# Optimization experiments

Hardware: AMD Instinct MI355X
Metric: run time of the kernel (lower is better)

The kernel has to match this reference:

```python
import jax, jax.numpy as jnp
import numpy as np

NUM_ORI = 20
DEGREE = 2
EPS = 1e-5

def _gelu(x):
    return jax.nn.gelu(x, approximate=False)

def _poly(x, degree=DEGREE):
    # PolynomialFeatures: concat of tensor powers 1..degree+1 of last dim
    feats = [x]
    cur = x
    for _ in range(degree):
        cur = (cur[..., :, None] * x[..., None, :]).reshape(x.shape[:-1] + (-1,))
        feats.append(cur)
    return jnp.concatenate(feats, axis=-1)

def setup_inputs():
    key = jax.random.key(0)
    ks = jax.random.split(key, 16)
    B, N, O, Cin, C, L = 1, 160, NUM_ORI, 16, 128, 2
    basis = C
    def w(k, shape, fan_in):
        return jax.random.normal(k, shape, jnp.float32) / np.sqrt(fan_in).astype(np.float32)
    return {
        "x": jax.random.normal(ks[0], (B, N, O, Cin), jnp.float32),
        "pos": jax.random.normal(ks[1], (B, N, 2), jnp.float32),
        "bw1": w(ks[2], (14, C), 14), "bb1": jnp.zeros((C,), jnp.float32),
        "bw2": w(ks[3], (C, basis), C), "bb2": jnp.zeros((basis,), jnp.float32),
        "fw1": w(ks[4], (3, C), 3), "fb1": jnp.zeros((C,), jnp.float32),
        "fw2": w(ks[5], (C, basis), C), "fb2": jnp.zeros((basis,), jnp.float32),
        "emb_w": w(ks[6], (Cin, C), Cin),
        "kernel_w": w(ks[7], (L, basis, C), basis),
        "fiber_w": w(ks[8], (L, basis, C), basis),
        "conv_b": jnp.zeros((L, C), jnp.float32),
        "ln_g": jnp.ones((L, C), jnp.float32), "ln_b": jnp.zeros((L, C), jnp.float32),
        "mlp_w1": w(ks[9], (L, C, 4 * C), C), "mlp_b1": jnp.zeros((L, 4 * C), jnp.float32),
        "mlp_w2": w(ks[10], (L, 4 * C, C), 4 * C), "mlp_b2": jnp.zeros((L, C), jnp.float32),
    }

def reference(x, pos, bw1, bb1, bw2, bb2, fw1, fb1, fw2, fb2, emb_w,
              kernel_w, fiber_w, conv_b, ln_g, ln_b, mlp_w1, mlp_b1, mlp_w2, mlp_b2):
    # uniform grid of orientations on the circle (GridGenerator(2, num_ori))
    theta = jnp.arange(NUM_ORI, dtype=jnp.float32) * (2.0 * jnp.pi / NUM_ORI)
    ori = jnp.stack([jnp.cos(theta), jnp.sin(theta)], axis=-1)              # [O,2]
    rel = pos[:, None, :, None, :] - pos[:, :, None, None, :]               # [B,M,N,1,2]
    inv1 = jnp.sum(rel * ori[None, None, None], axis=-1, keepdims=True)     # [B,M,N,O,1]
    inv2 = jnp.linalg.norm(rel - rel * inv1, axis=-1, keepdims=True)        # [B,M,N,O,1]
    spat = jnp.concatenate([inv1, inv2], axis=-1)                           # [B,M,N,O,2]
    kb = _gelu(_gelu(_poly(spat) @ bw1 + bb1) @ bw2 + bb2)                  # [B,M,N,O,basis]
    oi = jnp.sum(ori[:, None] * ori[None], axis=-1, keepdims=True)          # [P,O,1]
    fkb = _gelu(_gelu(_poly(oi) @ fw1 + fb1) @ fw2 + fb2)                   # [P,O,basis]
    h = x @ emb_w                                                           # [B,N,O,C]
    C = emb_w.shape[1]
    for l in range(kernel_w.shape[0]):
        kern = kb @ kernel_w[l]                                             # [B,M,N,O,C]
        fk = fkb @ fiber_w[l]                                               # [P,O,C]
        x1 = jnp.einsum('bnoc,bmnoc->bmoc', h, kern)                        # spatial conv
        x2 = jnp.einsum('bmoc,poc->bmpc', x1, fk) / C + conv_b[l]           # fiber conv (depthwise)
        mu = jnp.mean(x2, axis=-1, keepdims=True)
        var = jnp.var(x2, axis=-1, keepdims=True)
        xn = (x2 - mu) / jnp.sqrt(var + EPS) * ln_g[l] + ln_b[l]            # LayerNorm
        mid = _gelu(xn @ mlp_w1[l] + mlp_b1[l])                             # bottleneck MLP
        h = h + (mid @ mlp_w2[l] + mlp_b2[l])                               # residual (layer_scale=None)
    return h
```

## Files before the change

kernel.cpp:

```cpp
#include <hip/hip_runtime.h>
#include <math.h>

#define NORI 20
#define NPTS 160
#define CDIM 128
#define TWO_PI_OVER_O (6.28318530717958647692f / 20.0f)
#define SW 132
#define SAS 136
#define SCL 256.0f
#define ISCL 0.00390625f

typedef __attribute__((ext_vector_type(8))) _Float16 half8v;
typedef __attribute__((ext_vector_type(4))) float float4v;

__device__ __forceinline__ float vexp2(float x) {
    float r;
    asm("v_exp_f32 %0, %1" : "=v"(r) : "v"(x));
    return r;
}
__device__ __forceinline__ float vsqrt(float x) {
    float r;
    asm("v_sqrt_f32 %0, %1" : "=v"(r) : "v"(x));
    return r;
}

__device__ __forceinline__ float gelu_exact(float x) {
    float t  = 0.70710678118654752440f * x;
    float at = fabsf(t);
    float tau = __builtin_amdgcn_rcpf(fmaf(0.3275911f, at, 1.0f));
    float p = fmaf(1.061405429f, tau, -1.453152027f);
    p = fmaf(p, tau, 1.421413741f);
    p = fmaf(p, tau, -0.284496736f);
    p = fmaf(p, tau, 0.254829592f);
    p = p * tau;
    float e = vexp2(t * t * -1.44269504088896340736f);
    float erf_abs = fmaf(-p, e, 1.0f);
    float hx = 0.5f * x;
    return fmaf(fabsf(hx), erf_abs, hx);
}
__device__ __forceinline__ float4 ld4(const float* p) { return *(const float4*)p; }
__device__ __forceinline__ unsigned short f16b(float f) {
    _Float16 h = (_Float16)f;
    return __builtin_bit_cast(unsigned short, h);
}
__device__ __forceinline__ float f16tof(unsigned short u) {
    return (float)__builtin_bit_cast(_Float16, u);
}
__device__ __forceinline__ unsigned int pkrtz(float a, float b) {
    auto h = __builtin_amdgcn_cvt_pkrtz(a, b);
    return __builtin_bit_cast(unsigned int, h);
}

#define FMA4(d, s, v) { d.x += (s)*(v).x; d.y += (s)*(v).y; d.z += (s)*(v).z; d.w += (s)*(v).w; }
#define GELU4(d) { d.x = gelu_exact(d.x); d.y = gelu_exact(d.y); \
                   d.z = gelu_exact(d.z); d.w = gelu_exact(d.w); }

__global__ __launch_bounds__(128) void fk_kernel(
    const float* __restrict__ fw1, const float* __restrict__ fb1,
    const float* __restrict__ fw2, const float* __restrict__ fb2,
    const float* __restrict__ fiber_w, unsigned short* __restrict__ fk)
{
    __shared__ float s_u[CDIM];
    __shared__ float s_z[CDIM];
    int bid = blockIdx.x;
    int l = bid / 400;
    int rem = bid % 400;
    int p = rem / 20, o = rem % 20;
    int j = threadIdx.x;

    float t = cosf(TWO_PI_OVER_O * (float)(p - o));
    float f1 = t * t, f2 = f1 * t;

    float u = gelu_exact(t * fw1[j] + f1 * fw1[CDIM + j] + f2 * fw1[2 * CDIM + j] + fb1[j]);
    s_u[j] = u;
    __syncthreads();

    float z0 = 0.f, z1 = 0.f, z2 = 0.f, z3 = 0.f;
    for (int i = 0; i < CDIM; i += 4) {
        z0 += s_u[i    ] * fw2[(i    ) * CDIM + j];
        z1 += s_u[i + 1] * fw2[(i + 1) * CDIM + j];
        z2 += s_u[i + 2] * fw2[(i + 2) * CDIM + j];
        z3 += s_u[i + 3] * fw2[(i + 3) * CDIM + j];
    }
    float z = gelu_exact(((z0 + z1) + (z2 + z3)) + fb2[j]);
    s_z[j] = z;
    __syncthreads();

    const float* fw = fiber_w + l * CDIM * CDIM;
    float a0 = 0.f, a1 = 0.f, a2 = 0.f, a3 = 0.f;
    for (int i = 0; i < CDIM; i += 4) {
        a0 += s_z[i    ] * fw[(i    ) * CDIM + j];
        a1 += s_z[i + 1] * fw[(i + 1) * CDIM + j];
        a2 += s_z[i + 2] * fw[(i + 2) * CDIM + j];
        a3 += s_z[i + 3] * fw[(i + 3) * CDIM + j];
    }
    fk[bid * CDIM + j] = f16b((a0 + a1) + (a2 + a3));
}

__global__ __launch_bounds__(128) void h0_kernel(
    const float* __restrict__ x, const float* __restrict__ emb_w,
    float* __restrict__ h)
{
    int row = blockIdx.x;
    int j = threadIdx.x;
    const float* xr = x + row * 16;
    float acc = 0.f;
#pragma unroll
    for (int i = 0; i < 16; ++i) acc += xr[i] * emb_w[i * CDIM + j];
    h[row * CDIM + j] = acc;
}

__global__ __launch_bounds__(128) void wt_kernel(
    const float* __restrict__ bw2, const float* __restrict__ kernel_w,
    unsigned short* __restrict__ wt)
{
    int b = blockIdx.x;
    int mat = b >> 7, c = b & 127;
    const float* src = (mat == 0) ? bw2 : (kernel_w + (mat - 1) * CDIM * CDIM);
    int k = threadIdx.x;
    wt[(mat * CDIM + c) * CDIM + k] = f16b(src[k * CDIM + c]);
}

#define FOR_BANDS(X) X(0) X(1) X(2) X(3) X(4) X(5) X(6) X(7) X(8) X(9)

#define DECL_ACC(B) float4v acc##B = {0.f,0.f,0.f,0.f};

#define LDB(PTR, KT) (*(const half8v*)((PTR) + col0 * CDIM + (KT) * 32 + lh8))

#define LOADB(P, PTR) \
    half8v P##0 = LDB(PTR, 0); \
    half8v P##1 = LDB(PTR, 1); \
    half8v P##2 = LDB(PTR, 2); \
    half8v P##3 = LDB(PTR, 3);

#define G_BAND(B, P) { \
    const unsigned short* ar_ = s_act + (B) * 16 * SAS + abase; \
    half8v a0_ = *(const half8v*)(ar_); \
    half8v a1_ = *(const half8v*)(ar_ + 32); \
    half8v a2_ = *(const half8v*)(ar_ + 64); \
    half8v a3_ = *(const half8v*)(ar_ + 96); \
    acc##B = __builtin_amdgcn_mfma_f32_16x16x32_f16(a0_, P##0, acc##B, 0, 0, 0); \
    acc##B = __builtin_amdgcn_mfma_f32_16x16x32_f16(a1_, P##1, acc##B, 0, 0, 0); \
    acc##B = __builtin_amdgcn_mfma_f32_16x16x32_f16(a2_, P##2, acc##B, 0, 0, 0); \
    acc##B = __builtin_amdgcn_mfma_f32_16x16x32_f16(a3_, P##3, acc##B, 0, 0, 0); }

#define G1(B) G_BAND(B, bwf)
#define G2(B) G_BAND(B, kwf)

#define ZW_BAND(B) { \
    int rb_ = (B) * 16 + lh4; \
    s_act[(rb_ + 0) * SAS + col0] = f16b(gelu_exact(fmaf(SCL, acc##B.x, zb0)) * ISCL); \
    s_act[(rb_ + 1) * SAS + col0] = f16b(gelu_exact(fmaf(SCL, acc##B.y, zb0)) * ISCL); \
    s_act[(rb_ + 2) * SAS + col0] = f16b(gelu_exact(fmaf(SCL, acc##B.z, zb0)) * ISCL); \
    s_act[(rb_ + 3) * SAS + col0] = f16b(gelu_exact(fmaf(SCL, acc##B.w, zb0)) * ISCL); \
    acc##B = vzero; }

#define H_BAND(B) { \
    int nb_ = (B) * 16 + lh4; \
    xacc0 += acc##B.x * hb0[(nb_ + 0) * 2560]; \
    xacc0 += acc##B.y * hb0[(nb_ + 1) * 2560]; \
    xacc0 += acc##B.z * hb0[(nb_ + 2) * 2560]; \
    xacc0 += acc##B.w * hb0[(nb_ + 3) * 2560]; }

__global__ __launch_bounds__(512, 4) void x1_kernel(
    const float* __restrict__ pos, const float* __restrict__ h,
    const float* __restrict__ bw1, const float* __restrict__ bb1,
    const float* __restrict__ bb2,
    const unsigned short* __restrict__ wtb,
    const unsigned short* __restrict__ wtk,
    float* __restrict__ x1)
{
    __shared__ __align__(16) unsigned short s_act[160 * SAS];
    __shared__ float s_bw1[9 * SW];
    __shared__ float s_bb1[CDIM];

    const int tid = threadIdx.x;
    const int rg = tid & 31;
    const int cgv = tid >> 5;
    const int c0u = cgv << 3;

    if (tid < CDIM) {
        const int c = tid;
        s_bw1[0 * SW + c] = bw1[0 * CDIM + c];
        s_bw1[1 * SW + c] = bw1[1 * CDIM + c];
        s_bw1[2 * SW + c] = bw1[2 * CDIM + c];
        s_bw1[3 * SW + c] = bw1[3 * CDIM + c] + bw1[4 * CDIM + c];
        s_bw1[4 * SW + c] = bw1[5 * CDIM + c];
        s_bw1[5 * SW + c] = bw1[6 * CDIM + c];
        s_bw1[6 * SW + c] = bw1[7 * CDIM + c] + bw1[8 * CDIM + c] + bw1[10 * CDIM + c];
        s_bw1[7 * SW + c] = bw1[9 * CDIM + c] + bw1[11 * CDIM + c] + bw1[12 * CDIM + c];
        s_bw1[8 * SW + c] = bw1[13 * CDIM + c];
        s_bb1[c] = bb1[c];
    }

    const int m = blockIdx.x / NORI;
    const int o = blockIdx.x % NORI;
    const float th = TWO_PI_OVER_O * (float)o;
    const float ox = cosf(th), oy = sinf(th);
    const float pmx = pos[2 * m], pmy = pos[2 * m + 1];

    __syncthreads();

#pragma unroll
    for (int rr = 0; rr < 5; ++rr) {
        const int row = rr * 32 + rg;
        float rx = pos[2 * row] - pmx, ry = pos[2 * row + 1] - pmy;
        float ia = rx * ox + ry * oy;
        float ib = vsqrt(rx * rx + ry * ry) * fabsf(1.0f - ia);
        float q2a = ia * ia, q2m = ia * ib, q2b = ib * ib;
        float q3a = q2a * ia, q3m = q2a * ib, q3n = q2m * ib, q3b = q2b * ib;
        float4 ua = ld4(&s_bb1[c0u]);
        float4 ub = ld4(&s_bb1[c0u + 4]);
#define UF(I, S) { float4 wa_ = ld4(&s_bw1[(I) * SW + c0u]); \
                   float4 wb_ = ld4(&s_bw1[(I) * SW + c0u + 4]); \
                   FMA4(ua, S, wa_); FMA4(ub, S, wb_); }
        UF(0, ia) UF(1, ib) UF(2, q2a) UF(3, q2m) UF(4, q2b)
        UF(5, q3a) UF(6, q3m) UF(7, q3n) UF(8, q3b)
#undef UF
        GELU4(ua) GELU4(ub)
        uint4 up;
        up.x = pkrtz(ua.x * ISCL, ua.y * ISCL);
        up.y = pkrtz(ua.z * ISCL, ua.w * ISCL);
        up.z = pkrtz(ub.x * ISCL, ub.y * ISCL);
        up.w = pkrtz(ub.z * ISCL, ub.w * ISCL);
        *(uint4*)&s_act[row * SAS + c0u] = up;
    }

    const int lane = tid & 63;
    const int wv = tid >> 6;
    const int li = lane & 15;
    const int lh = lane >> 4;
    const int lh8 = lh << 3, lh4 = lh << 2;
    const int col0 = wv * 16 + li;
    const int abase = li * SAS + lh8;
    const float4v vzero = {0.f, 0.f, 0.f, 0.f};

    FOR_BANDS(DECL_ACC)
    LOADB(bwf, wtb)
    __syncthreads();

    FOR_BANDS(G1)
    __syncthreads();

    const float zb0 = bb2[col0];
    FOR_BANDS(ZW_BAND)
    LOADB(kwf, wtk)
    __syncthreads();

    FOR_BANDS(G2)

    const float* hb0 = h + o * CDIM + col0;
    float xacc0 = 0.f;
    FOR_BANDS(H_BAND)

    xacc0 += __shfl_xor(xacc0, 16, 64);
    xacc0 += __shfl_xor(xacc0, 32, 64);

    if (lane < 16)
        x1[(m * NORI + o) * CDIM + col0] = xacc0 * SCL;
}

__global__ __launch_bounds__(128) void mlp_kernel(
    const float* __restrict__ x1, const unsigned short* __restrict__ fk_l,
    const float* __restrict__ conv_b, const float* __restrict__ ln_g,
    const float* __restrict__ ln_b,
    const float* __restrict__ w1, const float* __restrict__ b1,
    const float* __restrict__ w2, const float* __restrict__ b2,
    float* __restrict__ h)
{
    __shared__ float s_xn[2][132];
    __shared__ float s_mid[2][520];
    __shared__ float s_s1[2][2], s_sq[2][2];

    const int c = threadIdx.x;
    const int m = blockIdx.x / 10, pg = blockIdx.x % 10;
    const int lane = c & 63, wid = c >> 6;

    float x1v[NORI];
#pragma unroll
    for (int o = 0; o < NORI; ++o) x1v[o] = x1[(m * NORI + o) * CDIM + c];

    float x2v[2];
#pragma unroll
    for (int rr = 0; rr < 2; ++rr) {
        int p = pg * 2 + rr;
        float x2 = 0.f;
#pragma unroll
        for (int o = 0; o < NORI; ++o) x2 += x1v[o] * f16tof(fk_l[(p * NORI + o) * CDIM + c]);
        x2 = x2 * (1.0f / 128.0f) + conv_b[c];
        x2v[rr] = x2;
        float s1 = x2, sq = x2 * x2;
        for (int off = 32; off; off >>= 1) {
            s1 += __shfl_down(s1, off, 64);
            sq += __shfl_down(sq, off, 64);
        }
        if (lane == 0) { s_s1[rr][wid] = s1; s_sq[rr][wid] = sq; }
    }
    __syncthreads();
#pragma unroll
    for (int rr = 0; rr < 2; ++rr) {
        float mu  = (s_s1[rr][0] + s_s1[rr][1]) * (1.0f / 128.0f);
        float var = (s_sq[rr][0] + s_sq[rr][1]) * (1.0f / 128.0f) - mu * mu;
        float xn = (x2v[rr] - mu) * rsqrtf(var + 1e-5f) * ln_g[c] + ln_b[c];
        s_xn[rr][c] = xn;
    }
    __syncthreads();

#pragma unroll
    for (int kq = 0; kq < 4; ++kq) {
        int k = kq * CDIM + c;
        float b = b1[k];
        float ac0 = b, ac1 = b;
        for (int i = 0; i < CDIM; ++i) {
            float w = w1[i * 512 + k];
            ac0 += s_xn[0][i] * w;
            ac1 += s_xn[1][i] * w;
        }
        s_mid[0][k] = gelu_exact(ac0);
        s_mid[1][k] = gelu_exact(ac1);
    }
    __syncthreads();

    float ao0 = 0.f, ao1 = 0.f;
    for (int k = 0; k < 512; ++k) {
        float w = w2[k * CDIM + c];
        ao0 += s_mid[0][k] * w;
        ao1 += s_mid[1][k] * w;
    }
    float bb = b2[c];
    h[(m * NORI + pg * 2 + 0) * CDIM + c] += ao0 + bb;
    h[(m * NORI + pg * 2 + 1) * CDIM + c] += ao1 + bb;
}

extern "C" void kernel_launch(void* const* d_in, const int* in_sizes, int n_in,
                              void* d_out, int out_size, void* d_ws, size_t ws_size,
                              hipStream_t stream)
{
    const float* x        = (const float*)d_in[0];
    const float* pos      = (const float*)d_in[1];
    const float* bw1      = (const float*)d_in[2];
    const float* bb1      = (const float*)d_in[3];
    const float* bw2      = (const float*)d_in[4];
    const float* bb2      = (const float*)d_in[5];
    const float* fw1      = (const float*)d_in[6];
    const float* fb1      = (const float*)d_in[7];
    const float* fw2      = (const float*)d_in[8];
    const float* fb2      = (const float*)d_in[9];
    const float* emb_w    = (const float*)d_in[10];
    const float* kernel_w = (const float*)d_in[11];
    const float* fiber_w  = (const float*)d_in[12];
    const float* conv_b   = (const float*)d_in[13];
    const float* ln_g     = (const float*)d_in[14];
    const float* ln_b     = (const float*)d_in[15];
    const float* mlp_w1   = (const float*)d_in[16];
    const float* mlp_b1   = (const float*)d_in[17];
    const float* mlp_w2   = (const float*)d_in[18];
    const float* mlp_b2   = (const float*)d_in[19];

    float* h = (float*)d_out;

    unsigned short* wt = (unsigned short*)d_ws;
    unsigned short* fk = wt + 3 * CDIM * CDIM;
    float* x1 = (float*)(fk + 2 * NORI * NORI * CDIM);

    wt_kernel<<<3 * CDIM, 128, 0, stream>>>(bw2, kernel_w, wt);
    fk_kernel<<<2 * NORI * NORI, 128, 0, stream>>>(fw1, fb1, fw2, fb2, fiber_w, fk);
    h0_kernel<<<NPTS * NORI, 128, 0, stream>>>(x, emb_w, h);

    for (int l = 0; l < 2; ++l) {
        x1_kernel<<<NPTS * NORI, 512, 0, stream>>>(
            pos, h, bw1, bb1, bb2, wt, wt + (1 + l) * CDIM * CDIM, x1);
        mlp_kernel<<<NPTS * NORI / 2, 128, 0, stream>>>(
            x1, fk + l * NORI * NORI * CDIM,
            conv_b + l * CDIM, ln_g + l * CDIM, ln_b + l * CDIM,
            mlp_w1 + l * CDIM * 4 * CDIM, mlp_b1 + l * 4 * CDIM,
            mlp_w2 + l * 4 * CDIM * CDIM, mlp_b2 + l * CDIM, h);
    }
}
```

Measured before the change: 311.9 us.

## Process ten orientation rows per MLP block to reuse weight loads

The MLP kernel now handles ten output orientations per block with 256 threads instead of two with 128. Each loaded w1/w2 weight is reused across ten or five rows held in shared memory, and the inner loops are unrolled by four with float4 shared reads. This cuts global weight traffic per output row by roughly a factor of five. In exchange the grid shrinks from 1600 to 320 blocks, and the larger shared-memory footprint and register count may lower occupancy.

```diff
diff --git a/kernel.cpp b/kernel.cpp
--- a/kernel.cpp
+++ b/kernel.cpp
@@ -260,7 +260,7 @@
         x1[(m * NORI + o) * CDIM + col0] = xacc0 * SCL;
 }
 
-__global__ __launch_bounds__(128) void mlp_kernel(
+__global__ __launch_bounds__(256, 2) void mlp_kernel(
     const float* __restrict__ x1, const unsigned short* __restrict__ fk_l,
     const float* __restrict__ conv_b, const float* __restrict__ ln_g,
     const float* __restrict__ ln_b,
@@ -268,68 +268,101 @@
     const float* __restrict__ w2, const float* __restrict__ b2,
     float* __restrict__ h)
 {
-    __shared__ float s_xn[2][132];
-    __shared__ float s_mid[2][520];
-    __shared__ float s_s1[2][2], s_sq[2][2];
-
-    const int c = threadIdx.x;
-    const int m = blockIdx.x / 10, pg = blockIdx.x % 10;
-    const int lane = c & 63, wid = c >> 6;
+    __shared__ float s_xn[10][132];
+    __shared__ float s_mid[10][520];
+    __shared__ float s_s1[2][5][2], s_sq[2][5][2];
+
+    const int tid = threadIdx.x;
+    const int m = blockIdx.x >> 1, ph = blockIdx.x & 1;
+    const int c = tid & 127;
+    const int pg2 = tid >> 7;
+    const int lane = tid & 63;
+    const int wig = (tid >> 6) & 1;
 
     float x1v[NORI];
 #pragma unroll
     for (int o = 0; o < NORI; ++o) x1v[o] = x1[(m * NORI + o) * CDIM + c];
 
-    float x2v[2];
-#pragma unroll
-    for (int rr = 0; rr < 2; ++rr) {
-        int p = pg * 2 + rr;
-        float x2 = 0.f;
-#pragma unroll
-        for (int o = 0; o < NORI; ++o) x2 += x1v[o] * f16tof(fk_l[(p * NORI + o) * CDIM + c]);
-        x2 = x2 * (1.0f / 128.0f) + conv_b[c];
-        x2v[rr] = x2;
-        float s1 = x2, sq = x2 * x2;
-        for (int off = 32; off; off >>= 1) {
-            s1 += __shfl_down(s1, off, 64);
-            sq += __shfl_down(sq, off, 64);
+    const float cb = conv_b[c], lg = ln_g[c], lb = ln_b[c];
+
+    float x2v[5];
+#pragma unroll
+    for (int j = 0; j < 5; ++j) {
+        const int p = ph * 10 + pg2 + 2 * j;
+        float acc = 0.f;
+#pragma unroll
+        for (int o = 0; o < NORI; ++o)
+            acc += x1v[o] * f16tof(fk_l[(p * NORI + o) * CDIM + c]);
+        x2v[j] = acc * (1.0f / 128.0f) + cb;
+    }
+
+    float s1v[5], sqv[5];
+#pragma unroll
+    for (int j = 0; j < 5; ++j) { s1v[j] = x2v[j]; sqv[j] = x2v[j] * x2v[j]; }
+    for (int off = 32; off; off >>= 1) {
+#pragma unroll
+        for (int j = 0; j < 5; ++j) {
+            s1v[j] += __shfl_down(s1v[j], off, 64);
+            sqv[j] += __shfl_down(sqv[j], off, 64);
         }
-        if (lane == 0) { s_s1[rr][wid] = s1; s_sq[rr][wid] = sq; }
-    }
-    __syncthreads();
-#pragma unroll
-    for (int rr = 0; rr < 2; ++rr) {
-        float mu  = (s_s1[rr][0] + s_s1[rr][1]) * (1.0f / 128.0f);
-        float var = (s_sq[rr][0] + s_sq[rr][1]) * (1.0f / 128.0f) - mu * mu;
-        float xn = (x2v[rr] - mu) * rsqrtf(var + 1e-5f) * ln_g[c] + ln_b[c];
-        s_xn[rr][c] = xn;
-    }
-    __syncthreads();
-
-#pragma unroll
-    for (int kq = 0; kq < 4; ++kq) {
-        int k = kq * CDIM + c;
-        float b = b1[k];
-        float ac0 = b, ac1 = b;
-        for (int i = 0; i < CDIM; ++i) {
-            float w = w1[i * 512 + k];
-            ac0 += s_xn[0][i] * w;
-            ac1 += s_xn[1][i] * w;
+    }
+    if (lane == 0) {
+#pragma unroll
+        for (int j = 0; j < 5; ++j) { s_s1[pg2][j][wig] = s1v[j]; s_sq[pg2][j][wig] = sqv[j]; }
+    }
+    __syncthreads();
+#pragma unroll
+    for (int j = 0; j < 5; ++j) {
+        const int pl = pg2 + 2 * j;
+        float mu  = (s_s1[pg2][j][0] + s_s1[pg2][j][1]) * (1.0f / 128.0f);
+        float var = (s_sq[pg2][j][0] + s_sq[pg2][j][1]) * (1.0f / 128.0f) - mu * mu;
+        s_xn[pl][c] = (x2v[j] - mu) * rsqrtf(var + 1e-5f) * lg + lb;
+    }
+    __syncthreads();
+
+    {
+        float a0[10], a1[10];
+#pragma unroll
+        for (int r = 0; r < 10; ++r) { a0[r] = 0.f; a1[r] = 0.f; }
+        const int k0 = tid, k1 = tid + 256;
+        for (int i4 = 0; i4 < 128; i4 += 4) {
+            float w00 = w1[(i4 + 0) * 512 + k0], w01 = w1[(i4 + 1) * 512 + k0];
+            float w02 = w1[(i4 + 2) * 512 + k0], w03 = w1[(i4 + 3) * 512 + k0];
+            float w10 = w1[(i4 + 0) * 512 + k1], w11 = w1[(i4 + 1) * 512 + k1];
+            float w12 = w1[(i4 + 2) * 512 + k1], w13 = w1[(i4 + 3) * 512 + k1];
+#pragma unroll
+            for (int r = 0; r < 10; ++r) {
+                float4 xr = ld4(&s_xn[r][i4]);
+                a0[r] = fmaf(xr.x, w00, fmaf(xr.y, w01, fmaf(xr.z, w02, fmaf(xr.w, w03, a0[r]))));
+                a1[r] = fmaf(xr.x, w10, fmaf(xr.y, w11, fmaf(xr.z, w12, fmaf(xr.w, w13, a1[r]))));
+            }
         }
-        s_mid[0][k] = gelu_exact(ac0);
-        s_mid[1][k] = gelu_exact(ac1);
-    }
-    __syncthreads();
-
-    float ao0 = 0.f, ao1 = 0.f;
-    for (int k = 0; k < 512; ++k) {
-        float w = w2[k * CDIM + c];
-        ao0 += s_mid[0][k] * w;
-        ao1 += s_mid[1][k] * w;
-    }
-    float bb = b2[c];
-    h[(m * NORI + pg * 2 + 0) * CDIM + c] += ao0 + bb;
-    h[(m * NORI + pg * 2 + 1) * CDIM + c] += ao1 + bb;
+        const float bk0 = b1[k0], bk1 = b1[k1];
+#pragma unroll
+        for (int r = 0; r < 10; ++r) {
+            s_mid[r][k0] = gelu_exact(a0[r] + bk0);
+            s_mid[r][k1] = gelu_exact(a1[r] + bk1);
+        }
+    }
+    __syncthreads();
+
+    float out0 = 0.f, out1 = 0.f, out2 = 0.f, out3 = 0.f, out4 = 0.f;
+    for (int k4 = 0; k4 < 512; k4 += 4) {
+        float wv0 = w2[(k4 + 0) * 128 + c], wv1 = w2[(k4 + 1) * 128 + c];
+        float wv2 = w2[(k4 + 2) * 128 + c], wv3 = w2[(k4 + 3) * 128 + c];
+#define M2ROW(OUT, J) { \
+        float4 mv = ld4(&s_mid[pg2 + 2 * (J)][k4]); \
+        OUT = fmaf(mv.x, wv0, fmaf(mv.y, wv1, fmaf(mv.z, wv2, fmaf(mv.w, wv3, OUT)))); }
+        M2ROW(out0, 0) M2ROW(out1, 1) M2ROW(out2, 2) M2ROW(out3, 3) M2ROW(out4, 4)
+#undef M2ROW
+    }
+    const float bb = b2[c];
+    float* hp = h + (m * NORI + ph * 10 + pg2) * CDIM + c;
+    hp[0 * 2 * CDIM] += out0 + bb;
+    hp[1 * 2 * CDIM] += out1 + bb;
+    hp[2 * 2 * CDIM] += out2 + bb;
+    hp[3 * 2 * CDIM] += out3 + bb;
+    hp[4 * 2 * CDIM] += out4 + bb;
 }
 
 extern "C" void kernel_launch(void* const* d_in, const int* in_sizes, int n_in,
@@ -370,7 +403,7 @@
     for (int l = 0; l < 2; ++l) {
         x1_kernel<<<NPTS * NORI, 512, 0, stream>>>(
             pos, h, bw1, bb1, bb2, wt, wt + (1 + l) * CDIM * CDIM, x1);
-        mlp_kernel<<<NPTS * NORI / 2, 128, 0, stream>>>(
+        mlp_kernel<<<NPTS * 2, 256, 0, stream>>>(
             x1, fk + l * NORI * NORI * CDIM,
             conv_b + l * CDIM, ln_g + l * CDIM, ln_b + l * CDIM,
             mlp_w1 + l * CDIM * 4 * CDIM, mlp_b1 + l * 4 * CDIM,
```

Measured after the change: 288.6 us. -7.5%, faster.
